# Optimization experiments

Measured on AMD Instinct MI355X. Metric: run time of the kernel, lower is better.

## Reference

```python
import jax, jax.numpy as jnp
import numpy as np

D_MODEL = 512
N_HEADS = 8
D_FF = 2048

def _linear_params(key, d_in, d_out):
    kw, kb = jax.random.split(key)
    bound = 1.0 / np.sqrt(d_in)
    W = jax.random.uniform(kw, (d_in, d_out), minval=-bound, maxval=bound, dtype=jnp.float32)
    b = jax.random.uniform(kb, (d_out,), minval=-bound, maxval=bound, dtype=jnp.float32)
    return W, b

def setup_inputs() -> dict:
    key = jax.random.key(0)
    ks = jax.random.split(key, 7)
    x = jax.random.normal(ks[0], (4, 2048, D_MODEL), dtype=jnp.float32)
    Wq, bq = _linear_params(ks[1], D_MODEL, D_MODEL)
    Wk, bk = _linear_params(ks[2], D_MODEL, D_MODEL)
    Wv, bv = _linear_params(ks[3], D_MODEL, D_MODEL)
    W1, b1 = _linear_params(ks[4], D_MODEL, D_FF)
    W2, b2 = _linear_params(ks[5], D_FF, D_MODEL)
    g1 = jnp.ones((D_MODEL,), jnp.float32); be1 = jnp.zeros((D_MODEL,), jnp.float32)
    g2 = jnp.ones((D_MODEL,), jnp.float32); be2 = jnp.zeros((D_MODEL,), jnp.float32)
    return {"x": x, "Wq": Wq, "bq": bq, "Wk": Wk, "bk": bk, "Wv": Wv, "bv": bv,
            "W1": W1, "b1": b1, "W2": W2, "b2": b2,
            "g1": g1, "be1": be1, "g2": g2, "be2": be2}

def _layernorm(x, g, b, eps=1e-5):
    mu = jnp.mean(x, axis=-1, keepdims=True)
    var = jnp.mean(jnp.square(x - mu), axis=-1, keepdims=True)
    return (x - mu) * jax.lax.rsqrt(var + eps) * g + b

def reference(x, Wq, bq, Wk, bk, Wv, bv, W1, b1, W2, b2, g1, be1, g2, be2):
    B, S, D = x.shape
    H = N_HEADS
    Dh = D // H
    residual = x
    xn = _layernorm(x, g1, be1)
    # [B,S,D] -> [B,H,S,Dh]
    q = (xn @ Wq + bq).reshape(B, S, H, Dh).transpose(0, 2, 1, 3)
    k = (xn @ Wk + bk).reshape(B, S, H, Dh).transpose(0, 2, 1, 3)
    v = (xn @ Wv + bv).reshape(B, S, H, Dh).transpose(0, 2, 1, 3)
    # sigmoid pointwise attention, scaled by sqrt(d_model) (not head dim)
    scores = jnp.einsum('bhsd,bhtd->bhst', q, k) / jnp.sqrt(jnp.float32(D))
    attn = jax.nn.sigmoid(scores)
    out = jnp.einsum('bhst,bhtd->bhsd', attn, v)
    out = out.transpose(0, 2, 1, 3).reshape(B, S, D)
    x = residual + out  # dropout=0 (eval)
    residual = x
    xn = _layernorm(x, g2, be2)
    ffn = jax.nn.relu(xn @ W1 + b1) @ W2 + b2
    return residual + ffn
```

## Files before the change

### kernel.cpp

```cpp
#include <hip/hip_runtime.h>
#include <hip/hip_bf16.h>
#include <math.h>

#define D_MODEL 512
#define N_HEADS 8
#define D_HEAD 64
#define D_FF 2048
#define SEQ 2048
#define BATCH 4
#define NTOK (BATCH * SEQ)
#define QSCALE 0.04419417382415922f
#define QSCALE_L2E (-QSCALE * 1.44269504089f)

typedef unsigned short ushort_t;
typedef __attribute__((ext_vector_type(8))) short short8;
typedef __attribute__((ext_vector_type(4))) short short4v;
typedef __attribute__((ext_vector_type(4))) float float4v;

static __device__ __forceinline__ ushort_t f2bf(float f) {
    union { float f; unsigned int i; } c; c.f = f;
    unsigned int i = c.i;
    unsigned int r = (i + 0x7FFFu + ((i >> 16) & 1u)) >> 16;
    return (ushort_t)r;
}

static __device__ __forceinline__ unsigned int pack2bf(float a, float b) {
    union { __hip_bfloat162 h; unsigned int u; } c;
    c.h = __float22bfloat162_rn(make_float2(a, b));
    return c.u;
}

static __device__ __forceinline__ float sig2(float x) {
    return __builtin_amdgcn_rcpf(1.0f + __builtin_amdgcn_exp2f(x));
}

__global__ __launch_bounds__(256) void k_prep_weights(const float* __restrict__ Wq,
                                                      const float* __restrict__ Wk,
                                                      const float* __restrict__ Wv,
                                                      const float* __restrict__ W1,
                                                      const float* __restrict__ W2,
                                                      ushort_t* __restrict__ Wqkvt,
                                                      ushort_t* __restrict__ W1t,
                                                      ushort_t* __restrict__ W2t) {
    __shared__ ushort_t tile[64][66];
    int bid = blockIdx.x;
    const float* src; ushort_t* dst; int K, N, tk, tn;
    if (bid < 192) {
        int m = bid >> 6, r = bid & 63;
        src = (m == 0) ? Wq : ((m == 1) ? Wk : Wv);
        dst = Wqkvt + (size_t)m * 512 * 512; K = 512; N = 512; tk = r >> 3; tn = r & 7;
    } else if (bid < 448) {
        int r = bid - 192; src = W1; dst = W1t; K = 512; N = 2048; tk = r >> 5; tn = r & 31;
    } else {
        int r = bid - 448; src = W2; dst = W2t; K = 2048; N = 512; tk = r >> 3; tn = r & 7;
    }
    int k0 = tk * 64, n0 = tn * 64;
    int rr = threadIdx.x >> 6, c = threadIdx.x & 63;
#pragma unroll
    for (int i = 0; i < 16; i++) {
        int row = i * 4 + rr;
        tile[row][c] = f2bf(src[(size_t)(k0 + row) * N + n0 + c]);
    }
    __syncthreads();
#pragma unroll
    for (int i = 0; i < 16; i++) {
        int row = i * 4 + rr;
        dst[(size_t)(n0 + row) * K + k0 + c] = tile[c][row];
    }
}

__global__ __launch_bounds__(256) void k_layernorm(const float* __restrict__ X,
                                                   const float* __restrict__ g,
                                                   const float* __restrict__ be,
                                                   ushort_t* __restrict__ Out) {
    int row  = blockIdx.x * 4 + (threadIdx.x >> 6);
    int lane = threadIdx.x & 63;
    const float* x = X + (size_t)row * D_MODEL + lane * 8;
    float4 v0 = ((const float4*)x)[0];
    float4 v1 = ((const float4*)x)[1];
    float vals[8] = {v0.x, v0.y, v0.z, v0.w, v1.x, v1.y, v1.z, v1.w};
    float s = 0.f, sq = 0.f;
#pragma unroll
    for (int j = 0; j < 8; j++) { s += vals[j]; sq += vals[j] * vals[j]; }
#pragma unroll
    for (int off = 32; off; off >>= 1) { s += __shfl_xor(s, off); sq += __shfl_xor(sq, off); }
    float mu  = s * (1.0f / D_MODEL);
    float var = sq * (1.0f / D_MODEL) - mu * mu;
    float inv = rsqrtf(var + 1e-5f);
    const float* gp  = g  + lane * 8;
    const float* bp  = be + lane * 8;
    float4 g0 = ((const float4*)gp)[0], g1v = ((const float4*)gp)[1];
    float4 b0 = ((const float4*)bp)[0], b1v = ((const float4*)bp)[1];
    float gs[8] = {g0.x, g0.y, g0.z, g0.w, g1v.x, g1v.y, g1v.z, g1v.w};
    float bs[8] = {b0.x, b0.y, b0.z, b0.w, b1v.x, b1v.y, b1v.z, b1v.w};
    ushort_t o[8];
#pragma unroll
    for (int j = 0; j < 8; j++) o[j] = f2bf((vals[j] - mu) * inv * gs[j] + bs[j]);
    ushort_t* op = Out + (size_t)row * D_MODEL + lane * 8;
    *(uint4*)op = *(uint4*)o;
}

static __device__ __forceinline__ void stage_tile(const ushort_t* __restrict__ G, int K,
                                                  ushort_t* L, int nchunks, int koff,
                                                  int w, int l) {
#pragma unroll
    for (int n = w; n < nchunks; n += 4) {
        const ushort_t* g = G + (size_t)(n * 16 + (l >> 2)) * K + koff + (l & 3) * 8;
        __builtin_amdgcn_global_load_lds((const __attribute__((address_space(1))) void*)g,
                                         (__attribute__((address_space(3))) void*)(L + n * 512),
                                         16, 0, 0);
    }
}

template <int JW>
static __device__ __forceinline__ void gemm_core2(const ushort_t* __restrict__ A,
                                                  const ushort_t* __restrict__ Bt,
                                                  int K, int m0, int n0,
                                                  ushort_t* As, ushort_t* Bs,
                                                  float4v acc[4][JW]) {
    const int BBUF = JW * 1024;
    int t = threadIdx.x, w = t >> 6, l = t & 63, q = l >> 4, lm = l & 15;
    int mb = (w & 1) * 64, nb = (w >> 1) * (JW * 16);
    const ushort_t* Ab = A + (size_t)m0 * K;
    const ushort_t* Bb = Bt + (size_t)n0 * K;
    int T = K >> 5;

    stage_tile(Ab, K, As, 8, 0, w, l);
    stage_tile(Bb, K, Bs, 2 * JW, 0, w, l);
    __syncthreads();

    for (int kt = 0; kt < T; kt++) {
        int cur = kt & 1;
        if (kt + 1 < T) {
            stage_tile(Ab, K, As + (1 - cur) * 4096, 8, (kt + 1) * 32, w, l);
            stage_tile(Bb, K, Bs + (1 - cur) * BBUF, 2 * JW, (kt + 1) * 32, w, l);
        }
        const ushort_t* asb = As + cur * 4096;
        const ushort_t* bsb = Bs + cur * BBUF;
        short8 a[4], b[JW];
#pragma unroll
        for (int i = 0; i < 4; i++) a[i] = *(const short8*)&asb[(mb + 16 * i + lm) * 32 + q * 8];
#pragma unroll
        for (int j = 0; j < JW; j++) b[j] = *(const short8*)&bsb[(nb + 16 * j + lm) * 32 + q * 8];
#pragma unroll
        for (int i = 0; i < 4; i++)
#pragma unroll
            for (int j = 0; j < JW; j++)
                acc[i][j] = __builtin_amdgcn_mfma_f32_16x16x32_bf16(a[i], b[j], acc[i][j], 0, 0, 0);
        __syncthreads();
    }
}

__global__ __launch_bounds__(256) void k_gemm_qkv(const ushort_t* __restrict__ A,
                                                  const ushort_t* __restrict__ Bt,
                                                  const float* __restrict__ bq,
                                                  const float* __restrict__ bk,
                                                  const float* __restrict__ bv,
                                                  ushort_t* __restrict__ qb,
                                                  ushort_t* __restrict__ kb,
                                                  ushort_t* __restrict__ vt) {
    __shared__ __align__(16) ushort_t As[8192];
    __shared__ __align__(16) ushort_t Bs[8192];
    int m0 = blockIdx.x * 128, n0 = blockIdx.y * 128;
    float4v acc[4][4];
#pragma unroll
    for (int i = 0; i < 4; i++)
#pragma unroll
        for (int j = 0; j < 4; j++) acc[i][j] = (float4v){0.f, 0.f, 0.f, 0.f};
    gemm_core2<4>(A, Bt, D_MODEL, m0, n0, As, Bs, acc);

    int t = threadIdx.x, w = t >> 6, l = t & 63, q = l >> 4, lm = l & 15;
    int mb = (w & 1) * 64, nb = (w >> 1) * 64;
    int mat = n0 >> 9, c0 = n0 & 511;
    const float* bias = (mat == 0) ? bq : ((mat == 1) ? bk : bv);
#pragma unroll
    for (int j = 0; j < 4; j++) {
        int cl = c0 + nb + 16 * j + lm;
        int hh = cl >> 6, dh = cl & 63;
        float bvv = bias[cl];
#pragma unroll
        for (int i = 0; i < 4; i++) {
            int mr0 = m0 + mb + 16 * i + q * 4;
            int bb = mr0 >> 11, ss0 = mr0 & (SEQ - 1);
            if (mat == 2) {
                union { ushort_t s[4]; uint2 v; } pk;
#pragma unroll
                for (int r = 0; r < 4; r++) pk.s[r] = f2bf(acc[i][j][r] + bvv);
                *(uint2*)&vt[((size_t)(bb * N_HEADS + hh) * D_HEAD + dh) * SEQ + ss0] = pk.v;
            } else {
                ushort_t* dst = (mat == 0) ? qb : kb;
                float sc = (mat == 0) ? QSCALE_L2E : 1.0f;
#pragma unroll
                for (int r = 0; r < 4; r++)
                    dst[((size_t)(bb * N_HEADS + hh) * SEQ + ss0 + r) * D_HEAD + dh] =
                        f2bf((acc[i][j][r] + bvv) * sc);
            }
        }
    }
}

__global__ __launch_bounds__(256) void k_gemm_ffn1(const ushort_t* __restrict__ A,
                                                   const ushort_t* __restrict__ Bt,
                                                   const float* __restrict__ b1,
                                                   ushort_t* __restrict__ hb) {
    __shared__ __align__(16) ushort_t As[8192];
    __shared__ __align__(16) ushort_t Bs[8192];
    int m0 = blockIdx.x * 128, n0 = blockIdx.y * 128;
    float4v acc[4][4];
#pragma unroll
    for (int i = 0; i < 4; i++)
#pragma unroll
        for (int j = 0; j < 4; j++) acc[i][j] = (float4v){0.f, 0.f, 0.f, 0.f};
    gemm_core2<4>(A, Bt, D_MODEL, m0, n0, As, Bs, acc);

    int t = threadIdx.x, w = t >> 6, l = t & 63, q = l >> 4, lm = l & 15;
    int mb = (w & 1) * 64, nb = (w >> 1) * 64;
#pragma unroll
    for (int j = 0; j < 4; j++) {
        int cl = n0 + nb + 16 * j + lm;
        float bvv = b1[cl];
#pragma unroll
        for (int i = 0; i < 4; i++) {
            int mr0 = m0 + mb + 16 * i + q * 4;
#pragma unroll
            for (int r = 0; r < 4; r++)
                hb[(size_t)(mr0 + r) * D_FF + cl] = f2bf(fmaxf(acc[i][j][r] + bvv, 0.f));
        }
    }
}

__global__ __launch_bounds__(256) void k_gemm_ffn2(const ushort_t* __restrict__ A,
                                                   const ushort_t* __restrict__ Bt,
                                                   const float* __restrict__ b2,
                                                   const float* __restrict__ res,
                                                   float* __restrict__ out) {
    __shared__ __align__(16) ushort_t As[8192];
    __shared__ __align__(16) ushort_t Bs[4096];
    int m0 = blockIdx.x * 128, n0 = blockIdx.y * 64;
    float4v acc[4][2];
#pragma unroll
    for (int i = 0; i < 4; i++)
#pragma unroll
        for (int j = 0; j < 2; j++) acc[i][j] = (float4v){0.f, 0.f, 0.f, 0.f};
    gemm_core2<2>(A, Bt, D_FF, m0, n0, As, Bs, acc);

    int t = threadIdx.x, w = t >> 6, l = t & 63, q = l >> 4, lm = l & 15;
    int mb = (w & 1) * 64, nb = (w >> 1) * 32;
#pragma unroll
    for (int j = 0; j < 2; j++) {
        int cl = n0 + nb + 16 * j + lm;
        float bvv = b2[cl];
#pragma unroll
        for (int i = 0; i < 4; i++) {
            int mr0 = m0 + mb + 16 * i + q * 4;
#pragma unroll
            for (int r = 0; r < 4; r++) {
                size_t idx = (size_t)(mr0 + r) * D_MODEL + cl;
                out[idx] = acc[i][j][r] + bvv + res[idx];
            }
        }
    }
}

__global__ __launch_bounds__(512) void k_attention(const ushort_t* __restrict__ Q,
                                                   const ushort_t* __restrict__ Kb,
                                                   const ushort_t* __restrict__ Vt,
                                                   const float* __restrict__ X,
                                                   float* __restrict__ Y) {
    __shared__ __align__(16) char smem[36864];
    ushort_t* Ks = (ushort_t*)smem;
    ushort_t* Vs = (ushort_t*)(smem + 18432);
    float*  Osum = (float*)smem;

    int bh = blockIdx.y;
    int b = bh >> 3, h = bh & 7;
    size_t base = (size_t)bh * SEQ * D_HEAD;
    int s0 = blockIdx.x * 128;
    int t = threadIdx.x, w = t >> 6, l = t & 63, q = l >> 4, lm = l & 15;
    int g = w >> 1, th = w & 1;
    int srow = t >> 3, sc = (t & 7) * 8;

    short8 qf[2][2];
#pragma unroll
    for (int nt = 0; nt < 2; nt++)
#pragma unroll
        for (int kc = 0; kc < 2; kc++) {
            const ushort_t* qg = Q + base + (size_t)(s0 + 32 * g + 16 * nt + lm) * D_HEAD + kc * 32 + q * 8;
            uint4 u = *(const uint4*)qg;
            qf[nt][kc] = *(const short8*)&u;
        }

    float4v o[2][4];
#pragma unroll
    for (int nt = 0; nt < 2; nt++)
#pragma unroll
        for (int dj = 0; dj < 4; dj++) o[nt][dj] = (float4v){0.f, 0.f, 0.f, 0.f};

    uint4 kr, vr;
    const ushort_t* kg0 = Kb + base + (size_t)srow * D_HEAD + sc;
    const ushort_t* vg0 = Vt + base + (size_t)srow * SEQ + sc;

    kr = *(const uint4*)(kg0); vr = *(const uint4*)(vg0);
    *(uint4*)&Ks[srow * 72 + sc] = kr; *(uint4*)&Vs[srow * 72 + sc] = vr;
    kr = *(const uint4*)(kg0 + 64 * D_HEAD); vr = *(const uint4*)(vg0 + 64);
    __syncthreads();

    for (int tt = 0; tt < SEQ / 64; tt++) {
        int cur = tt & 1;
        const ushort_t* ksb = Ks + cur * 4608;
        const ushort_t* vsb = Vs + cur * 4608;
        short8 kf[2][2];
#pragma unroll
        for (int mt = 0; mt < 2; mt++)
#pragma unroll
            for (int kc = 0; kc < 2; kc++)
                kf[mt][kc] = *(const short8*)&ksb[(32 * th + 16 * mt + lm) * 72 + kc * 32 + q * 8];
        float4v st[2][2];
#pragma unroll
        for (int mt = 0; mt < 2; mt++)
#pragma unroll
            for (int nt = 0; nt < 2; nt++) st[mt][nt] = (float4v){0.f, 0.f, 0.f, 0.f};
#pragma unroll
        for (int kc = 0; kc < 2; kc++)
#pragma unroll
            for (int mt = 0; mt < 2; mt++)
#pragma unroll
                for (int nt = 0; nt < 2; nt++)
                    st[mt][nt] = __builtin_amdgcn_mfma_f32_16x16x32_bf16(kf[mt][kc], qf[nt][kc], st[mt][nt], 0, 0, 0);
        short4v pf[2][2];
#pragma unroll
        for (int mt = 0; mt < 2; mt++)
#pragma unroll
            for (int nt = 0; nt < 2; nt++) {
                union { unsigned int u[2]; short4v v; } pk;
                pk.u[0] = pack2bf(sig2(st[mt][nt][0]), sig2(st[mt][nt][1]));
                pk.u[1] = pack2bf(sig2(st[mt][nt][2]), sig2(st[mt][nt][3]));
                pf[mt][nt] = pk.v;
            }
#pragma unroll
        for (int mt = 0; mt < 2; mt++) {
            short4v vf[4];
#pragma unroll
            for (int dj = 0; dj < 4; dj++)
                vf[dj] = *(const short4v*)&vsb[(16 * dj + lm) * 72 + 32 * th + 16 * mt + 4 * q];
#pragma unroll
            for (int dj = 0; dj < 4; dj++)
#pragma unroll
                for (int nt = 0; nt < 2; nt++)
                    o[nt][dj] = __builtin_amdgcn_mfma_f32_16x16x16bf16_1k(vf[dj], pf[mt][nt], o[nt][dj], 0, 0, 0);
        }
        if (tt + 1 < SEQ / 64) {
            int nxt = 1 - cur;
            *(uint4*)&Ks[nxt * 4608 + srow * 72 + sc] = kr;
            *(uint4*)&Vs[nxt * 4608 + srow * 72 + sc] = vr;
            if (tt + 2 < SEQ / 64) {
                kr = *(const uint4*)(kg0 + (size_t)(tt + 2) * 64 * D_HEAD);
                vr = *(const uint4*)(vg0 + (tt + 2) * 64);
            }
        }
        __syncthreads();
    }

    __syncthreads();
    if (th == 0) {
#pragma unroll
        for (int nt = 0; nt < 2; nt++)
#pragma unroll
            for (int dj = 0; dj < 4; dj++) {
                float4v v = o[nt][dj];
                *(float4*)&Osum[(32 * g + 16 * nt + lm) * 68 + 16 * dj + 4 * q] =
                    make_float4(v[0], v[1], v[2], v[3]);
            }
    }
    __syncthreads();
    if (th == 1) {
#pragma unroll
        for (int nt = 0; nt < 2; nt++)
#pragma unroll
            for (int dj = 0; dj < 4; dj++) {
                float* p = &Osum[(32 * g + 16 * nt + lm) * 68 + 16 * dj + 4 * q];
                float4 old = *(float4*)p;
                float4v v = o[nt][dj];
                *(float4*)p = make_float4(old.x + v[0], old.y + v[1], old.z + v[2], old.w + v[3]);
            }
    }
    __syncthreads();

    {
        int row = t >> 2, c0 = (t & 3) * 16;
        size_t gro = ((size_t)(b * SEQ + s0 + row)) * D_MODEL + h * D_HEAD + c0;
        const float* xp = X + gro;
        float* yp = Y + gro;
        const float* os = &Osum[row * 68 + c0];
#pragma unroll
        for (int i = 0; i < 4; i++) {
            float4 xv = *(const float4*)(xp + i * 4);
            float4 ov = *(const float4*)(os + i * 4);
            float4 rr;
            rr.x = xv.x + ov.x; rr.y = xv.y + ov.y;
            rr.z = xv.z + ov.z; rr.w = xv.w + ov.w;
            *(float4*)(yp + i * 4) = rr;
        }
    }
}

extern "C" void kernel_launch(void* const* d_in, const int* in_sizes, int n_in,
                              void* d_out, int out_size, void* d_ws, size_t ws_size,
                              hipStream_t stream) {
    const float* x   = (const float*)d_in[0];
    const float* Wq  = (const float*)d_in[1];
    const float* bq  = (const float*)d_in[2];
    const float* Wk  = (const float*)d_in[3];
    const float* bk  = (const float*)d_in[4];
    const float* Wv  = (const float*)d_in[5];
    const float* bv  = (const float*)d_in[6];
    const float* W1  = (const float*)d_in[7];
    const float* b1  = (const float*)d_in[8];
    const float* W2  = (const float*)d_in[9];
    const float* b2  = (const float*)d_in[10];
    const float* g1  = (const float*)d_in[11];
    const float* be1 = (const float*)d_in[12];
    const float* g2  = (const float*)d_in[13];
    const float* be2 = (const float*)d_in[14];
    float* out = (float*)d_out;

    char* p = (char*)d_ws;
    ushort_t* xn    = (ushort_t*)p; p += (size_t)NTOK * D_MODEL * 2;
    ushort_t* yn    = (ushort_t*)p; p += (size_t)NTOK * D_MODEL * 2;
    float*    y     = (float*)p;    p += (size_t)NTOK * D_MODEL * 4;
    ushort_t* qb    = (ushort_t*)p; p += (size_t)NTOK * D_MODEL * 2;
    ushort_t* kb    = (ushort_t*)p; p += (size_t)NTOK * D_MODEL * 2;
    ushort_t* vt    = (ushort_t*)p; p += (size_t)NTOK * D_MODEL * 2;
    ushort_t* hb    = (ushort_t*)p; p += (size_t)NTOK * D_FF * 2;
    ushort_t* Wqkvt = (ushort_t*)p; p += (size_t)3 * D_MODEL * D_MODEL * 2;
    ushort_t* W1t   = (ushort_t*)p; p += (size_t)D_MODEL * D_FF * 2;
    ushort_t* W2t   = (ushort_t*)p; p += (size_t)D_FF * D_MODEL * 2;

    k_prep_weights<<<704, 256, 0, stream>>>(Wq, Wk, Wv, W1, W2, Wqkvt, W1t, W2t);

    k_layernorm<<<NTOK / 4, 256, 0, stream>>>(x, g1, be1, xn);

    dim3 gq(NTOK / 128, (3 * D_MODEL) / 128);
    k_gemm_qkv<<<gq, 256, 0, stream>>>(xn, Wqkvt, bq, bk, bv, qb, kb, vt);

    dim3 ga(SEQ / 128, BATCH * N_HEADS);
    k_attention<<<ga, 512, 0, stream>>>(qb, kb, vt, x, y);

    k_layernorm<<<NTOK / 4, 256, 0, stream>>>(y, g2, be2, yn);

    dim3 g1d(NTOK / 128, D_FF / 128);
    k_gemm_ffn1<<<g1d, 256, 0, stream>>>(yn, W1t, b1, hb);
    dim3 g2d(NTOK / 128, D_MODEL / 64);
    k_gemm_ffn2<<<g2d, 256, 0, stream>>>(hb, W2t, b2, y, out);
}
```

Before: 241.6 us.

## Split attention key tiles across four warps per query group with atomic reduction

Each attention block now handles 64 query rows instead of 128, with 4 warps per 32-query group each taking 16 keys of every 64-key tile rather than 2 warps taking 32. The grid doubles to raise occupancy and parallelism. Partial outputs from three warps are combined into shared memory with per-element atomicAdd instead of a single read-modify-write. In exchange, each K/V tile loaded into LDS is reused by fewer queries, so total K/V traffic doubles, and the shared-memory atomics add reduction cost.

```diff
diff --git a/kernel.cpp b/kernel.cpp
--- a/kernel.cpp
+++ b/kernel.cpp
@@ -275,9 +275,9 @@
     int bh = blockIdx.y;
     int b = bh >> 3, h = bh & 7;
     size_t base = (size_t)bh * SEQ * D_HEAD;
-    int s0 = blockIdx.x * 128;
+    int s0 = blockIdx.x * 64;
     int t = threadIdx.x, w = t >> 6, l = t & 63, q = l >> 4, lm = l & 15;
-    int g = w >> 1, th = w & 1;
+    int g = w >> 2, th = w & 3;
     int srow = t >> 3, sc = (t & 7) * 8;
 
     short8 qf[2][2];
@@ -309,45 +309,36 @@
         int cur = tt & 1;
         const ushort_t* ksb = Ks + cur * 4608;
         const ushort_t* vsb = Vs + cur * 4608;
-        short8 kf[2][2];
-#pragma unroll
-        for (int mt = 0; mt < 2; mt++)
-#pragma unroll
-            for (int kc = 0; kc < 2; kc++)
-                kf[mt][kc] = *(const short8*)&ksb[(32 * th + 16 * mt + lm) * 72 + kc * 32 + q * 8];
-        float4v st[2][2];
-#pragma unroll
-        for (int mt = 0; mt < 2; mt++)
-#pragma unroll
-            for (int nt = 0; nt < 2; nt++) st[mt][nt] = (float4v){0.f, 0.f, 0.f, 0.f};
+        short8 kf[2];
 #pragma unroll
         for (int kc = 0; kc < 2; kc++)
-#pragma unroll
-            for (int mt = 0; mt < 2; mt++)
+            kf[kc] = *(const short8*)&ksb[(16 * th + lm) * 72 + kc * 32 + q * 8];
+        float4v st[2];
+#pragma unroll
+        for (int nt = 0; nt < 2; nt++) st[nt] = (float4v){0.f, 0.f, 0.f, 0.f};
+#pragma unroll
+        for (int kc = 0; kc < 2; kc++)
+#pragma unroll
+            for (int nt = 0; nt < 2; nt++)
+                st[nt] = __builtin_amdgcn_mfma_f32_16x16x32_bf16(kf[kc], qf[nt][kc], st[nt], 0, 0, 0);
+        short4v pf[2];
+#pragma unroll
+        for (int nt = 0; nt < 2; nt++) {
+            union { unsigned int u[2]; short4v v; } pk;
+            pk.u[0] = pack2bf(sig2(st[nt][0]), sig2(st[nt][1]));
+            pk.u[1] = pack2bf(sig2(st[nt][2]), sig2(st[nt][3]));
+            pf[nt] = pk.v;
+        }
+        {
+            short4v vf[4];
+#pragma unroll
+            for (int dj = 0; dj < 4; dj++)
+                vf[dj] = *(const short4v*)&vsb[(16 * dj + lm) * 72 + 16 * th + 4 * q];
+#pragma unroll
+            for (int dj = 0; dj < 4; dj++)
 #pragma unroll
                 for (int nt = 0; nt < 2; nt++)
-                    st[mt][nt] = __builtin_amdgcn_mfma_f32_16x16x32_bf16(kf[mt][kc], qf[nt][kc], st[mt][nt], 0, 0, 0);
-        short4v pf[2][2];
-#pragma unroll
-        for (int mt = 0; mt < 2; mt++)
-#pragma unroll
-            for (int nt = 0; nt < 2; nt++) {
-                union { unsigned int u[2]; short4v v; } pk;
-                pk.u[0] = pack2bf(sig2(st[mt][nt][0]), sig2(st[mt][nt][1]));
-                pk.u[1] = pack2bf(sig2(st[mt][nt][2]), sig2(st[mt][nt][3]));
-                pf[mt][nt] = pk.v;
-            }
-#pragma unroll
-        for (int mt = 0; mt < 2; mt++) {
-            short4v vf[4];
-#pragma unroll
-            for (int dj = 0; dj < 4; dj++)
-                vf[dj] = *(const short4v*)&vsb[(16 * dj + lm) * 72 + 32 * th + 16 * mt + 4 * q];
-#pragma unroll
-            for (int dj = 0; dj < 4; dj++)
-#pragma unroll
-                for (int nt = 0; nt < 2; nt++)
-                    o[nt][dj] = __builtin_amdgcn_mfma_f32_16x16x16bf16_1k(vf[dj], pf[mt][nt], o[nt][dj], 0, 0, 0);
+                    o[nt][dj] = __builtin_amdgcn_mfma_f32_16x16x16bf16_1k(vf[dj], pf[nt], o[nt][dj], 0, 0, 0);
         }
         if (tt + 1 < SEQ / 64) {
             int nxt = 1 - cur;
@@ -361,7 +352,6 @@
         __syncthreads();
     }
 
-    __syncthreads();
     if (th == 0) {
 #pragma unroll
         for (int nt = 0; nt < 2; nt++)
@@ -373,27 +363,29 @@
             }
     }
     __syncthreads();
-    if (th == 1) {
+    if (th != 0) {
 #pragma unroll
         for (int nt = 0; nt < 2; nt++)
 #pragma unroll
             for (int dj = 0; dj < 4; dj++) {
                 float* p = &Osum[(32 * g + 16 * nt + lm) * 68 + 16 * dj + 4 * q];
-                float4 old = *(float4*)p;
                 float4v v = o[nt][dj];
-                *(float4*)p = make_float4(old.x + v[0], old.y + v[1], old.z + v[2], old.w + v[3]);
+                atomicAdd(p + 0, v[0]);
+                atomicAdd(p + 1, v[1]);
+                atomicAdd(p + 2, v[2]);
+                atomicAdd(p + 3, v[3]);
             }
     }
     __syncthreads();
 
     {
-        int row = t >> 2, c0 = (t & 3) * 16;
+        int row = t >> 3, c0 = (t & 7) * 8;
         size_t gro = ((size_t)(b * SEQ + s0 + row)) * D_MODEL + h * D_HEAD + c0;
         const float* xp = X + gro;
         float* yp = Y + gro;
         const float* os = &Osum[row * 68 + c0];
 #pragma unroll
-        for (int i = 0; i < 4; i++) {
+        for (int i = 0; i < 2; i++) {
             float4 xv = *(const float4*)(xp + i * 4);
             float4 ov = *(const float4*)(os + i * 4);
             float4 rr;
@@ -443,7 +435,7 @@
     dim3 gq(NTOK / 128, (3 * D_MODEL) / 128);
     k_gemm_qkv<<<gq, 256, 0, stream>>>(xn, Wqkvt, bq, bk, bv, qb, kb, vt);
 
-    dim3 ga(SEQ / 128, BATCH * N_HEADS);
+    dim3 ga(SEQ / 64, BATCH * N_HEADS);
     k_attention<<<ga, 512, 0, stream>>>(qb, kb, vt, x, y);
 
     k_layernorm<<<NTOK / 4, 256, 0, stream>>>(y, g2, be2, yn);
```

Result: slower. 300.8 us (+24.5%).

## Double the attention KV tile to 128 keys and add MFMA priority hints

Applied to the files above, without the earlier changes.

The attention kernel now stages 128 keys per iteration instead of 64, which halves the number of loop iterations and block-wide barriers. The double-buffered shared memory grows to about 70 KB, with the V layout padded to 136 columns. s_setprio is raised around the MFMA sections so these waves get scheduling priority. A redundant trailing __syncthreads is removed. The larger LDS footprint and more live registers may reduce how many blocks fit on a CU at once.

```diff
diff --git a/kernel.cpp b/kernel.cpp
--- a/kernel.cpp
+++ b/kernel.cpp
@@ -262,15 +262,19 @@
     }
 }
 
-__global__ __launch_bounds__(512) void k_attention(const ushort_t* __restrict__ Q,
-                                                   const ushort_t* __restrict__ Kb,
-                                                   const ushort_t* __restrict__ Vt,
-                                                   const float* __restrict__ X,
-                                                   float* __restrict__ Y) {
-    __shared__ __align__(16) char smem[36864];
+__global__ __launch_bounds__(512, 4) void k_attention(const ushort_t* __restrict__ Q,
+                                                      const ushort_t* __restrict__ Kb,
+                                                      const ushort_t* __restrict__ Vt,
+                                                      const float* __restrict__ X,
+                                                      float* __restrict__ Y) {
+    __shared__ __align__(16) char smem[71680];
     ushort_t* Ks = (ushort_t*)smem;
-    ushort_t* Vs = (ushort_t*)(smem + 18432);
+    ushort_t* Vs = (ushort_t*)(smem + 36864);
     float*  Osum = (float*)smem;
+
+    const int KBUF = 128 * 72;
+    const int VBUF = 64 * 136;
+    const int NIT  = SEQ / 128;
 
     int bh = blockIdx.y;
     int b = bh >> 3, h = bh & 7;
@@ -279,6 +283,7 @@
     int t = threadIdx.x, w = t >> 6, l = t & 63, q = l >> 4, lm = l & 15;
     int g = w >> 1, th = w & 1;
     int srow = t >> 3, sc = (t & 7) * 8;
+    int srowV = t >> 4, scV = (t & 15) * 8;
 
     short8 qf[2][2];
 #pragma unroll
@@ -296,72 +301,88 @@
 #pragma unroll
         for (int dj = 0; dj < 4; dj++) o[nt][dj] = (float4v){0.f, 0.f, 0.f, 0.f};
 
-    uint4 kr, vr;
     const ushort_t* kg0 = Kb + base + (size_t)srow * D_HEAD + sc;
-    const ushort_t* vg0 = Vt + base + (size_t)srow * SEQ + sc;
-
-    kr = *(const uint4*)(kg0); vr = *(const uint4*)(vg0);
-    *(uint4*)&Ks[srow * 72 + sc] = kr; *(uint4*)&Vs[srow * 72 + sc] = vr;
-    kr = *(const uint4*)(kg0 + 64 * D_HEAD); vr = *(const uint4*)(vg0 + 64);
+    const ushort_t* vg0 = Vt + base + (size_t)srowV * SEQ + scV;
+
+    uint4 kr0, kr1, vr0, vr1;
+    kr0 = *(const uint4*)(kg0);
+    kr1 = *(const uint4*)(kg0 + 64 * D_HEAD);
+    vr0 = *(const uint4*)(vg0);
+    vr1 = *(const uint4*)(vg0 + 32 * SEQ);
+    *(uint4*)&Ks[srow * 72 + sc]          = kr0;
+    *(uint4*)&Ks[(srow + 64) * 72 + sc]   = kr1;
+    *(uint4*)&Vs[srowV * 136 + scV]       = vr0;
+    *(uint4*)&Vs[(srowV + 32) * 136 + scV] = vr1;
+    kr0 = *(const uint4*)(kg0 + 128 * D_HEAD);
+    kr1 = *(const uint4*)(kg0 + 192 * D_HEAD);
+    vr0 = *(const uint4*)(vg0 + 128);
+    vr1 = *(const uint4*)(vg0 + 32 * SEQ + 128);
     __syncthreads();
 
-    for (int tt = 0; tt < SEQ / 64; tt++) {
+    for (int tt = 0; tt < NIT; tt++) {
         int cur = tt & 1;
-        const ushort_t* ksb = Ks + cur * 4608;
-        const ushort_t* vsb = Vs + cur * 4608;
-        short8 kf[2][2];
-#pragma unroll
-        for (int mt = 0; mt < 2; mt++)
+        const ushort_t* ksb = Ks + cur * KBUF;
+        const ushort_t* vsb = Vs + cur * VBUF;
+
+        short4v pf[4][2];
+#pragma unroll
+        for (int mt = 0; mt < 4; mt++) {
+            short8 kf[2];
 #pragma unroll
             for (int kc = 0; kc < 2; kc++)
-                kf[mt][kc] = *(const short8*)&ksb[(32 * th + 16 * mt + lm) * 72 + kc * 32 + q * 8];
-        float4v st[2][2];
-#pragma unroll
-        for (int mt = 0; mt < 2; mt++)
-#pragma unroll
-            for (int nt = 0; nt < 2; nt++) st[mt][nt] = (float4v){0.f, 0.f, 0.f, 0.f};
-#pragma unroll
-        for (int kc = 0; kc < 2; kc++)
-#pragma unroll
-            for (int mt = 0; mt < 2; mt++)
+                kf[kc] = *(const short8*)&ksb[(64 * th + 16 * mt + lm) * 72 + kc * 32 + q * 8];
+            float4v st[2];
+            st[0] = (float4v){0.f, 0.f, 0.f, 0.f};
+            st[1] = (float4v){0.f, 0.f, 0.f, 0.f};
+            __builtin_amdgcn_s_setprio(1);
+#pragma unroll
+            for (int kc = 0; kc < 2; kc++)
 #pragma unroll
                 for (int nt = 0; nt < 2; nt++)
-                    st[mt][nt] = __builtin_amdgcn_mfma_f32_16x16x32_bf16(kf[mt][kc], qf[nt][kc], st[mt][nt], 0, 0, 0);
-        short4v pf[2][2];
-#pragma unroll
-        for (int mt = 0; mt < 2; mt++)
+                    st[nt] = __builtin_amdgcn_mfma_f32_16x16x32_bf16(kf[kc], qf[nt][kc], st[nt], 0, 0, 0);
+            __builtin_amdgcn_s_setprio(0);
 #pragma unroll
             for (int nt = 0; nt < 2; nt++) {
                 union { unsigned int u[2]; short4v v; } pk;
-                pk.u[0] = pack2bf(sig2(st[mt][nt][0]), sig2(st[mt][nt][1]));
-                pk.u[1] = pack2bf(sig2(st[mt][nt][2]), sig2(st[mt][nt][3]));
+                pk.u[0] = pack2bf(sig2(st[nt][0]), sig2(st[nt][1]));
+                pk.u[1] = pack2bf(sig2(st[nt][2]), sig2(st[nt][3]));
                 pf[mt][nt] = pk.v;
             }
-#pragma unroll
-        for (int mt = 0; mt < 2; mt++) {
+        }
+
+        __builtin_amdgcn_s_setprio(1);
+#pragma unroll
+        for (int mt = 0; mt < 4; mt++) {
             short4v vf[4];
 #pragma unroll
             for (int dj = 0; dj < 4; dj++)
-                vf[dj] = *(const short4v*)&vsb[(16 * dj + lm) * 72 + 32 * th + 16 * mt + 4 * q];
+                vf[dj] = *(const short4v*)&vsb[(16 * dj + lm) * 136 + 64 * th + 16 * mt + 4 * q];
 #pragma unroll
             for (int dj = 0; dj < 4; dj++)
 #pragma unroll
                 for (int nt = 0; nt < 2; nt++)
                     o[nt][dj] = __builtin_amdgcn_mfma_f32_16x16x16bf16_1k(vf[dj], pf[mt][nt], o[nt][dj], 0, 0, 0);
         }
-        if (tt + 1 < SEQ / 64) {
+        __builtin_amdgcn_s_setprio(0);
+
+        if (tt + 1 < NIT) {
             int nxt = 1 - cur;
-            *(uint4*)&Ks[nxt * 4608 + srow * 72 + sc] = kr;
-            *(uint4*)&Vs[nxt * 4608 + srow * 72 + sc] = vr;
-            if (tt + 2 < SEQ / 64) {
-                kr = *(const uint4*)(kg0 + (size_t)(tt + 2) * 64 * D_HEAD);
-                vr = *(const uint4*)(vg0 + (tt + 2) * 64);
+            *(uint4*)&Ks[nxt * KBUF + srow * 72 + sc]           = kr0;
+            *(uint4*)&Ks[nxt * KBUF + (srow + 64) * 72 + sc]    = kr1;
+            *(uint4*)&Vs[nxt * VBUF + srowV * 136 + scV]        = vr0;
+            *(uint4*)&Vs[nxt * VBUF + (srowV + 32) * 136 + scV] = vr1;
+            if (tt + 2 < NIT) {
+                size_t ko = (size_t)(tt + 2) * 128 * D_HEAD;
+                size_t vo = (size_t)(tt + 2) * 128;
+                kr0 = *(const uint4*)(kg0 + ko);
+                kr1 = *(const uint4*)(kg0 + ko + 64 * D_HEAD);
+                vr0 = *(const uint4*)(vg0 + vo);
+                vr1 = *(const uint4*)(vg0 + vo + 32 * SEQ);
             }
         }
         __syncthreads();
     }
 
-    __syncthreads();
     if (th == 0) {
 #pragma unroll
         for (int nt = 0; nt < 2; nt++)
```

Result: slower. 249.5 us (+3.3%).
